# Performance work log

Hardware: AMD Instinct MI355X
Metric: run time of the kernel (lower is better)

## Reference

```python
import jax, jax.numpy as jnp
import numpy as np

N = 50000
E = 800000
D = 128
EPS = 1e-5


def _init_lin(key, d_in, d_out):
    return (jax.random.normal(key, (d_out, d_in), dtype=jnp.float32) / np.sqrt(d_in)).astype(jnp.float32)


def setup_inputs() -> dict:
    key = jax.random.key(0)
    ks = jax.random.split(key, 16)
    x = jax.random.normal(ks[0], (N, D), dtype=jnp.float32)
    edge_index = jax.random.randint(ks[1], (2, E), 0, N, dtype=jnp.int32)
    inp = {"x": x, "edge_index": edge_index}
    # 3 SAGEConv layers: Wl (neighbor/aggr path, with bias), Wr (root path, no bias)
    for i in range(3):
        inp[f"Wl{i}"] = _init_lin(ks[2 + 3 * i], D, D)
        inp[f"bl{i}"] = jnp.zeros((D,), dtype=jnp.float32)
        inp[f"Wr{i}"] = _init_lin(ks[3 + 3 * i], D, D)
    # single LayerNorm (applied after conv0 only, since len(norms)=num_layers-2=1)
    inp["ln_g"] = jnp.ones((D,), dtype=jnp.float32)
    inp["ln_b"] = jnp.zeros((D,), dtype=jnp.float32)
    return inp


def _sage_conv(x, src, dst, Wl, bl, Wr):
    # sum-aggregate source features into destination nodes: [N, D]
    agg = jax.ops.segment_sum(x[src], dst, num_segments=N)
    return agg @ Wl.T + bl + x @ Wr.T


def _layernorm(h, g, b):
    mu = jnp.mean(h, axis=-1, keepdims=True)
    var = jnp.mean(jnp.square(h - mu), axis=-1, keepdims=True)
    return (h - mu) * jax.lax.rsqrt(var + EPS) * g + b


def reference(x, edge_index, Wl0, bl0, Wr0, Wl1, bl1, Wr1, Wl2, bl2, Wr2, ln_g, ln_b):
    src, dst = edge_index[0], edge_index[1]
    # layer 0: conv -> layernorm -> relu (dropout inactive in eval)
    h = _sage_conv(x, src, dst, Wl0, bl0, Wr0)
    h = jax.nn.relu(_layernorm(h, ln_g, ln_b))
    # layer 1: conv -> relu (no norm: i >= len(norms))
    h = jax.nn.relu(_sage_conv(h, src, dst, Wl1, bl1, Wr1))
    # layer 2: final conv, no activation
    return _sage_conv(h, src, dst, Wl2, bl2, Wr2)
```

## Files before the change

### kernel.cpp

```cpp
#include <hip/hip_runtime.h>
#include <hip/hip_bf16.h>

#define NN 50000
#define EE 800000
#define DD 128
#define SLOTS 64
#define PART 6250
#define GEMM_BLOCKS 391
#define PLACE_BLOCKS 4096
#define STRIPE 1563
#define POISON ((int)0xAAAAAAAA)

typedef __attribute__((ext_vector_type(8))) short short8;
typedef __attribute__((ext_vector_type(4))) float floatx4;
typedef __attribute__((ext_vector_type(4))) unsigned short ushort4_t;

__device__ __forceinline__ short f2bf(float f) {
  union { float f; unsigned u; } c; c.f = f;
  unsigned r = c.u + 0x7FFFu + ((c.u >> 16) & 1u);
  return (short)(r >> 16);
}
__device__ __forceinline__ float bf2f(short s) {
  union { unsigned u; float f; } c; c.u = ((unsigned)(unsigned short)s) << 16;
  return c.f;
}
__device__ __forceinline__ unsigned pk(float a, float b) {
  return ((unsigned)(unsigned short)f2bf(a)) | (((unsigned)(unsigned short)f2bf(b)) << 16);
}

__global__ __launch_bounds__(256) void place_k(
    const int* __restrict__ srcE, const int* __restrict__ dstE,
    int* __restrict__ fill, unsigned short* __restrict__ srcSorted,
    const float* __restrict__ W0, const float* __restrict__ W1,
    const float* __restrict__ W2, const float* __restrict__ W3,
    const float* __restrict__ W4, const float* __restrict__ W5,
    short* __restrict__ Wbf, int* __restrict__ Udummy) {
  int b = blockIdx.x;
  if (b < 384) {
    int i = b * 256 + threadIdx.x;
    int mat = i >> 14, local = i & 16383;
    const float* W;
    switch (mat) {
      case 0: W = W0; break;
      case 1: W = W1; break;
      case 2: W = W2; break;
      case 3: W = W3; break;
      case 4: W = W4; break;
      default: W = W5; break;
    }
    int r = local >> 7, c = local & 127;
    int idx = r * DD + (((c >> 3) ^ (r & 15)) << 3) + (c & 7);
    Wbf[(mat << 14) + idx] = f2bf(W[local]);
    if (b == 0 && threadIdx.x < 64) Udummy[threadIdx.x] = 0;
  }
  int p = b & 7;
  int stripe = b >> 3;
  int base = stripe * STRIPE;
  for (int i = threadIdx.x; i < STRIPE; i += 256) {
    int e = base + i;
    if (e < EE) {
      int d = dstE[e];
      int s = srcE[e];
      if ((d & 7) == p) {
        int slot = atomicAdd(&fill[p * PART + (d >> 3)], 1) - POISON;
        if (slot >= 0 && slot < SLOTS)
          srcSorted[(size_t)d * SLOTS + slot] = (unsigned short)s;
      }
    }
  }
}

template <int BF16IN, int VBF16>
__global__ __launch_bounds__(512) void dual_gemm(
    const void* __restrict__ Ain, const short* __restrict__ Wpair,
    const float* __restrict__ bias,
    short* __restrict__ U, void* __restrict__ V)
{
  __shared__ __align__(16) short lw[2 * DD * DD];
  int t = threadIdx.x;
  {
    const short8* gp = (const short8*)Wpair;
    short8* lp = (short8*)lw;
#pragma unroll
    for (int i = 0; i < 8; ++i) lp[t + i * 512] = gp[t + i * 512];
  }

  int wave = t >> 6, lane = t & 63;
  int m = lane & 15, q = lane >> 4;
  int lrow = wave * 16 + m;
  int node = blockIdx.x * 128 + lrow;
  int ar = node < NN ? node : NN - 1;

  short8 af[4];
  if (BF16IN) {
    const short* H = (const short*)Ain + (size_t)ar * DD;
#pragma unroll
    for (int kc = 0; kc < 4; ++kc) af[kc] = *(const short8*)(H + kc * 32 + q * 8);
  } else {
    const floatx4* ap = (const floatx4*)((const float*)Ain + (size_t)ar * DD);
#pragma unroll
    for (int kc = 0; kc < 4; ++kc) {
      floatx4 p0 = ap[kc * 8 + q * 2];
      floatx4 p1 = ap[kc * 8 + q * 2 + 1];
      short8 s;
      s[0] = f2bf(p0[0]); s[1] = f2bf(p0[1]); s[2] = f2bf(p0[2]); s[3] = f2bf(p0[3]);
      s[4] = f2bf(p1[0]); s[5] = f2bf(p1[1]); s[6] = f2bf(p1[2]); s[7] = f2bf(p1[3]);
      af[kc] = s;
    }
  }
  __syncthreads();

  uint2 uacc[8];
  uint2 vaccb[8];
  floatx4 vaccf[8];
#pragma unroll
  for (int ct = 0; ct < 8; ++ct) {
    floatx4 au = {0.f, 0.f, 0.f, 0.f}, av = {0.f, 0.f, 0.f, 0.f};
    int colq = ct * 16 + q * 4;
    const short* pl = &lw[(ct * 16 + m) * DD];
    const short* pr = &lw[DD * DD + (ct * 16 + m) * DD];
#pragma unroll
    for (int kc = 0; kc < 4; ++kc) {
      int pos = (((kc * 4 + q) ^ m) << 3);
      short8 bl_ = *(const short8*)(pl + pos);
      short8 br_ = *(const short8*)(pr + pos);
      au = __builtin_amdgcn_mfma_f32_16x16x32_bf16(bl_, af[kc], au, 0, 0, 0);
      av = __builtin_amdgcn_mfma_f32_16x16x32_bf16(br_, af[kc], av, 0, 0, 0);
    }
    floatx4 bv = *(const floatx4*)(bias + colq);
    uacc[ct].x = pk(au[0], au[1]);
    uacc[ct].y = pk(au[2], au[3]);
    if (VBF16) {
      vaccb[ct].x = pk(av[0] + bv[0], av[1] + bv[1]);
      vaccb[ct].y = pk(av[2] + bv[2], av[3] + bv[3]);
    } else {
      floatx4 vv = {av[0] + bv[0], av[1] + bv[1], av[2] + bv[2], av[3] + bv[3]};
      vaccf[ct] = vv;
    }
  }
  __syncthreads();

  int base = blockIdx.x * 128;
  if (VBF16) {
#pragma unroll
    for (int ct = 0; ct < 8; ++ct) {
      int p = (ct * 4 + q) ^ m;
      *(uint2*)(lw + lrow * 128 + p * 4) = uacc[ct];
      *(uint2*)(lw + 16384 + lrow * 128 + p * 4) = vaccb[ct];
    }
    __syncthreads();
#pragma unroll
    for (int it = 0; it < 8; ++it) {
      int f = it * 512 + t;
      int row = f >> 5, gi = f & 31;
      int nd = base + row;
      if (nd < NN) {
        int p = gi ^ (row & 15);
        *(uint2*)(U + (size_t)nd * DD + gi * 4) =
            *(const uint2*)(lw + row * 128 + p * 4);
        *(uint2*)((short*)V + (size_t)nd * DD + gi * 4) =
            *(const uint2*)(lw + 16384 + row * 128 + p * 4);
      }
    }
  } else {
#pragma unroll
    for (int ct = 0; ct < 8; ++ct) {
      int p = (ct * 4 + q) ^ m;
      *(uint2*)(lw + lrow * 128 + p * 4) = uacc[ct];
    }
    __syncthreads();
#pragma unroll
    for (int it = 0; it < 8; ++it) {
      int f = it * 512 + t;
      int row = f >> 5, gi = f & 31;
      int nd = base + row;
      if (nd < NN) {
        int p = gi ^ (row & 15);
        *(uint2*)(U + (size_t)nd * DD + gi * 4) =
            *(const uint2*)(lw + row * 128 + p * 4);
      }
    }
    __syncthreads();
    float* lf = (float*)lw;
#pragma unroll
    for (int ct = 0; ct < 8; ++ct) {
      int p = (ct * 4 + q) ^ m;
      *(floatx4*)(lf + lrow * 128 + p * 4) = vaccf[ct];
    }
    __syncthreads();
#pragma unroll
    for (int it = 0; it < 8; ++it) {
      int f = it * 512 + t;
      int row = f >> 5, gi = f & 31;
      int nd = base + row;
      if (nd < NN) {
        int p = gi ^ (row & 15);
        *(floatx4*)((float*)V + (size_t)nd * DD + gi * 4) =
            *(const floatx4*)(lf + row * 128 + p * 4);
      }
    }
  }
}

template <int MODE>
__global__ __launch_bounds__(256) void agg_fuse(
    const short* __restrict__ U, const unsigned short* __restrict__ srcSorted,
    const int* __restrict__ fill, const short* __restrict__ Vbf,
    float* __restrict__ Vf, short* __restrict__ H,
    const float* __restrict__ g, const float* __restrict__ b)
{
  int node = blockIdx.x * 4 + (threadIdx.x >> 6);
  int lane = threadIdx.x & 63;
  int c = lane & 15, r = lane >> 4;
  int coff = c << 3;

  int deg = fill[(node & 7) * PART + (node >> 3)] - POISON;
  deg = deg < SLOTS ? deg : SLOTS;
  const unsigned short* seg = srcSorted + (size_t)node * SLOTS;

  float acc[8] = {0.f, 0.f, 0.f, 0.f, 0.f, 0.f, 0.f, 0.f};
  int nbatch = (deg + 15) >> 4;
  for (int bb = 0; bb < nbatch; ++bb) {
    int s0 = bb * 16 + (r << 2);
    ushort4_t idx = *(const ushort4_t*)(seg + s0);
    int ra0 = (s0 + 0) < deg ? (int)idx[0] : NN;
    int ra1 = (s0 + 1) < deg ? (int)idx[1] : NN;
    int ra2 = (s0 + 2) < deg ? (int)idx[2] : NN;
    int ra3 = (s0 + 3) < deg ? (int)idx[3] : NN;
    short8 v0 = *(const short8*)(U + ((size_t)ra0 << 7) + coff);
    short8 v1 = *(const short8*)(U + ((size_t)ra1 << 7) + coff);
    short8 v2 = *(const short8*)(U + ((size_t)ra2 << 7) + coff);
    short8 v3 = *(const short8*)(U + ((size_t)ra3 << 7) + coff);
#pragma unroll
    for (int j = 0; j < 8; ++j)
      acc[j] += (bf2f(v0[j]) + bf2f(v1[j])) + (bf2f(v2[j]) + bf2f(v3[j]));
  }
#pragma unroll
  for (int j = 0; j < 8; ++j) {
    acc[j] += __shfl_xor(acc[j], 16, 64);
    acc[j] += __shfl_xor(acc[j], 32, 64);
  }

  if (MODE == 0) {
    short8 vv = *(const short8*)(Vbf + ((size_t)node << 7) + coff);
#pragma unroll
    for (int j = 0; j < 8; ++j) acc[j] += bf2f(vv[j]);
    float s = 0.f;
#pragma unroll
    for (int j = 0; j < 8; ++j) s += acc[j];
    s += __shfl_xor(s, 1, 64); s += __shfl_xor(s, 2, 64);
    s += __shfl_xor(s, 4, 64); s += __shfl_xor(s, 8, 64);
    float mu = s * (1.0f / 128.0f);
    float q2 = 0.f;
#pragma unroll
    for (int j = 0; j < 8; ++j) { float d = acc[j] - mu; q2 += d * d; }
    q2 += __shfl_xor(q2, 1, 64); q2 += __shfl_xor(q2, 2, 64);
    q2 += __shfl_xor(q2, 4, 64); q2 += __shfl_xor(q2, 8, 64);
    float rstd = rsqrtf(q2 * (1.0f / 128.0f) + 1e-5f);
    floatx4 g0 = *(const floatx4*)(g + coff), g1 = *(const floatx4*)(g + coff + 4);
    floatx4 b0 = *(const floatx4*)(b + coff), b1 = *(const floatx4*)(b + coff + 4);
    float o[8];
#pragma unroll
    for (int j = 0; j < 4; ++j) {
      o[j]     = (acc[j]     - mu) * rstd * g0[j] + b0[j];
      o[4 + j] = (acc[4 + j] - mu) * rstd * g1[j] + b1[j];
    }
#pragma unroll
    for (int j = 0; j < 8; ++j) o[j] = o[j] > 0.f ? o[j] : 0.f;
    if (r == 0) {
      uint4 pkt = {pk(o[0], o[1]), pk(o[2], o[3]), pk(o[4], o[5]), pk(o[6], o[7])};
      *(uint4*)(H + ((size_t)node << 7) + coff) = pkt;
    }
  } else if (MODE == 1) {
    if (r == 0) {
      short8 vv = *(const short8*)(Vbf + ((size_t)node << 7) + coff);
#pragma unroll
      for (int j = 0; j < 8; ++j) {
        acc[j] += bf2f(vv[j]);
        acc[j] = acc[j] > 0.f ? acc[j] : 0.f;
      }
      uint4 pkt = {pk(acc[0], acc[1]), pk(acc[2], acc[3]),
                   pk(acc[4], acc[5]), pk(acc[6], acc[7])};
      *(uint4*)(H + ((size_t)node << 7) + coff) = pkt;
    }
  } else {
    if (r == 0) {
      float* vp = Vf + ((size_t)node << 7) + coff;
      floatx4 a0 = ((const floatx4*)vp)[0];
      floatx4 a1 = ((const floatx4*)vp)[1];
      floatx4 o0 = {acc[0] + a0[0], acc[1] + a0[1], acc[2] + a0[2], acc[3] + a0[3]};
      floatx4 o1 = {acc[4] + a1[0], acc[5] + a1[1], acc[6] + a1[2], acc[7] + a1[3]};
      ((floatx4*)vp)[0] = o0;
      ((floatx4*)vp)[1] = o1;
    }
  }
}

extern "C" void kernel_launch(void* const* d_in, const int* in_sizes, int n_in,
                              void* d_out, int out_size, void* d_ws, size_t ws_size,
                              hipStream_t stream) {
  const float* x   = (const float*)d_in[0];
  const int*   ei  = (const int*)d_in[1];
  const int* src = ei;
  const int* dst = ei + EE;
  const float* Wl0 = (const float*)d_in[2];
  const float* bl0 = (const float*)d_in[3];
  const float* Wr0 = (const float*)d_in[4];
  const float* Wl1 = (const float*)d_in[5];
  const float* bl1 = (const float*)d_in[6];
  const float* Wr1 = (const float*)d_in[7];
  const float* Wl2 = (const float*)d_in[8];
  const float* bl2 = (const float*)d_in[9];
  const float* Wr2 = (const float*)d_in[10];
  const float* lng = (const float*)d_in[11];
  const float* lnb = (const float*)d_in[12];

  short* Vbf = (short*)d_out;
  float* Vf  = (float*)d_out;

  short* U   = (short*)d_ws;
  short* Hb  = U + (size_t)(NN + 1) * DD;
  short* Wbf = Hb + (size_t)NN * DD;
  unsigned short* srcS = (unsigned short*)(Wbf + 6 * DD * DD);
  int* fill  = (int*)(srcS + (size_t)NN * SLOTS);

  dim3 blk(256);
  dim3 gblk(512);

  place_k<<<PLACE_BLOCKS, blk, 0, stream>>>(src, dst, fill, srcS,
                                            Wl0, Wr0, Wl1, Wr1, Wl2, Wr2,
                                            Wbf, (int*)(U + (size_t)NN * DD));

  dual_gemm<0, 1><<<GEMM_BLOCKS, gblk, 0, stream>>>(
      x, Wbf + 0 * 2 * DD * DD, bl0, U, Vbf);
  agg_fuse<0><<<NN / 4, blk, 0, stream>>>(U, srcS, fill, Vbf, Vf, Hb, lng, lnb);

  dual_gemm<1, 1><<<GEMM_BLOCKS, gblk, 0, stream>>>(
      Hb, Wbf + 1 * 2 * DD * DD, bl1, U, Vbf);
  agg_fuse<1><<<NN / 4, blk, 0, stream>>>(U, srcS, fill, Vbf, Vf, Hb, lng, lnb);

  dual_gemm<1, 0><<<GEMM_BLOCKS, gblk, 0, stream>>>(
      Hb, Wbf + 2 * 2 * DD * DD, bl2, U, Vf);
  agg_fuse<2><<<NN / 4, blk, 0, stream>>>(U, srcS, fill, Vbf, Vf, Hb, lng, lnb);
}
```

Baseline: 266.5 us.

## Fuse layer-0 GEMM with edge placement kernel and use nontemporal loads

```diff
diff --git a/kernel.cpp b/kernel.cpp
--- a/kernel.cpp
+++ b/kernel.cpp
@@ -7,8 +7,8 @@
 #define SLOTS 64
 #define PART 6250
 #define GEMM_BLOCKS 391
-#define PLACE_BLOCKS 4096
-#define STRIPE 1563
+#define PLACE_BLOCKS 2048
+#define STRIPE2 3125
 #define POISON ((int)0xAAAAAAAA)
 
 typedef __attribute__((ext_vector_type(8))) short short8;
@@ -28,51 +28,124 @@
   return ((unsigned)(unsigned short)f2bf(a)) | (((unsigned)(unsigned short)f2bf(b)) << 16);
 }
 
-__global__ __launch_bounds__(256) void place_k(
+__global__ __launch_bounds__(512) void gemm0_place(
+    const float* __restrict__ x,
+    const float* __restrict__ Wl0, const float* __restrict__ Wr0,
+    const float* __restrict__ bias,
+    short* __restrict__ U, short* __restrict__ Vbf,
     const int* __restrict__ srcE, const int* __restrict__ dstE,
     int* __restrict__ fill, unsigned short* __restrict__ srcSorted,
-    const float* __restrict__ W0, const float* __restrict__ W1,
-    const float* __restrict__ W2, const float* __restrict__ W3,
-    const float* __restrict__ W4, const float* __restrict__ W5,
-    short* __restrict__ Wbf, int* __restrict__ Udummy) {
-  int b = blockIdx.x;
-  if (b < 384) {
-    int i = b * 256 + threadIdx.x;
-    int mat = i >> 14, local = i & 16383;
-    const float* W;
-    switch (mat) {
-      case 0: W = W0; break;
-      case 1: W = W1; break;
-      case 2: W = W2; break;
-      case 3: W = W3; break;
-      case 4: W = W4; break;
-      default: W = W5; break;
-    }
-    int r = local >> 7, c = local & 127;
-    int idx = r * DD + (((c >> 3) ^ (r & 15)) << 3) + (c & 7);
-    Wbf[(mat << 14) + idx] = f2bf(W[local]);
-    if (b == 0 && threadIdx.x < 64) Udummy[threadIdx.x] = 0;
-  }
-  int p = b & 7;
-  int stripe = b >> 3;
-  int base = stripe * STRIPE;
-  for (int i = threadIdx.x; i < STRIPE; i += 256) {
-    int e = base + i;
-    if (e < EE) {
-      int d = dstE[e];
-      int s = srcE[e];
+    const float* __restrict__ Wl1, const float* __restrict__ Wr1,
+    const float* __restrict__ Wl2, const float* __restrict__ Wr2,
+    short* __restrict__ Wbf, int* __restrict__ Udummy)
+{
+  __shared__ __align__(16) short lw[2 * DD * DD];
+  int t = threadIdx.x;
+
+  if (blockIdx.x >= GEMM_BLOCKS) {
+    int b = blockIdx.x - GEMM_BLOCKS;
+    if (b < 128) {
+      int i = b * 512 + t;
+      int mat = i >> 14, local = i & 16383;
+      const float* W = (mat == 0) ? Wl1 : (mat == 1) ? Wr1 : (mat == 2) ? Wl2 : Wr2;
+      int r = local >> 7, c = local & 127;
+      int idx = r * DD + (((c >> 3) ^ (r & 15)) << 3) + (c & 7);
+      Wbf[(mat << 14) + idx] = f2bf(W[local]);
+      if (b == 0 && t < 64) Udummy[t] = 0;
+    }
+    int p = b & 7;
+    int stripe = b >> 3;
+    int base = stripe * STRIPE2;
+    for (int i = t; i < STRIPE2; i += 512) {
+      int e = base + i;
+      int d = __builtin_nontemporal_load(dstE + e);
+      int s = __builtin_nontemporal_load(srcE + e);
       if ((d & 7) == p) {
         int slot = atomicAdd(&fill[p * PART + (d >> 3)], 1) - POISON;
         if (slot >= 0 && slot < SLOTS)
           srcSorted[(size_t)d * SLOTS + slot] = (unsigned short)s;
       }
     }
-  }
-}
-
-template <int BF16IN, int VBF16>
+    return;
+  }
+
+  for (int i = t; i < DD * DD; i += 512) {
+    int r = i >> 7, c = i & 127;
+    int idx = r * DD + (((c >> 3) ^ (r & 15)) << 3) + (c & 7);
+    lw[idx] = f2bf(Wl0[i]);
+    lw[DD * DD + idx] = f2bf(Wr0[i]);
+  }
+
+  int wave = t >> 6, lane = t & 63;
+  int m = lane & 15, q = lane >> 4;
+  int lrow = wave * 16 + m;
+  int node = blockIdx.x * 128 + lrow;
+  int ar = node < NN ? node : NN - 1;
+
+  short8 af[4];
+  {
+    const floatx4* ap = (const floatx4*)(x + (size_t)ar * DD);
+#pragma unroll
+    for (int kc = 0; kc < 4; ++kc) {
+      floatx4 p0 = ap[kc * 8 + q * 2];
+      floatx4 p1 = ap[kc * 8 + q * 2 + 1];
+      short8 s;
+      s[0] = f2bf(p0[0]); s[1] = f2bf(p0[1]); s[2] = f2bf(p0[2]); s[3] = f2bf(p0[3]);
+      s[4] = f2bf(p1[0]); s[5] = f2bf(p1[1]); s[6] = f2bf(p1[2]); s[7] = f2bf(p1[3]);
+      af[kc] = s;
+    }
+  }
+  __syncthreads();
+
+  uint2 uacc[8], vaccb[8];
+#pragma unroll
+  for (int ct = 0; ct < 8; ++ct) {
+    floatx4 au = {0.f, 0.f, 0.f, 0.f}, av = {0.f, 0.f, 0.f, 0.f};
+    int colq = ct * 16 + q * 4;
+    const short* pl = &lw[(ct * 16 + m) * DD];
+    const short* pr = &lw[DD * DD + (ct * 16 + m) * DD];
+#pragma unroll
+    for (int kc = 0; kc < 4; ++kc) {
+      int pos = (((kc * 4 + q) ^ m) << 3);
+      short8 bl_ = *(const short8*)(pl + pos);
+      short8 br_ = *(const short8*)(pr + pos);
+      au = __builtin_amdgcn_mfma_f32_16x16x32_bf16(bl_, af[kc], au, 0, 0, 0);
+      av = __builtin_amdgcn_mfma_f32_16x16x32_bf16(br_, af[kc], av, 0, 0, 0);
+    }
+    floatx4 bv = *(const floatx4*)(bias + colq);
+    uacc[ct].x = pk(au[0], au[1]);
+    uacc[ct].y = pk(au[2], au[3]);
+    vaccb[ct].x = pk(av[0] + bv[0], av[1] + bv[1]);
+    vaccb[ct].y = pk(av[2] + bv[2], av[3] + bv[3]);
+  }
+  __syncthreads();
+
+  int base = blockIdx.x * 128;
+#pragma unroll
+  for (int ct = 0; ct < 8; ++ct) {
+    int p = (ct * 4 + q) ^ m;
+    *(uint2*)(lw + lrow * 128 + p * 4) = uacc[ct];
+    *(uint2*)(lw + 16384 + lrow * 128 + p * 4) = vaccb[ct];
+  }
+  __syncthreads();
+#pragma unroll
+  for (int it = 0; it < 8; ++it) {
+    int f = it * 512 + t;
+    int row = f >> 5, gi = f & 31;
+    int nd = base + row;
+    if (nd < NN) {
+      int p = gi ^ (row & 15);
+      *(uint2*)(U + (size_t)nd * DD + gi * 4) =
+          *(const uint2*)(lw + row * 128 + p * 4);
+      *(uint2*)(Vbf + (size_t)nd * DD + gi * 4) =
+          *(const uint2*)(lw + 16384 + row * 128 + p * 4);
+    }
+  }
+}
+
+template <int VBF16>
 __global__ __launch_bounds__(512) void dual_gemm(
-    const void* __restrict__ Ain, const short* __restrict__ Wpair,
+    const short* __restrict__ Ain, const short* __restrict__ Wpair,
     const float* __restrict__ bias,
     short* __restrict__ U, void* __restrict__ V)
 {
@@ -92,26 +165,14 @@
   int ar = node < NN ? node : NN - 1;
 
   short8 af[4];
-  if (BF16IN) {
-    const short* H = (const short*)Ain + (size_t)ar * DD;
+  {
+    const short* H = Ain + (size_t)ar * DD;
 #pragma unroll
     for (int kc = 0; kc < 4; ++kc) af[kc] = *(const short8*)(H + kc * 32 + q * 8);
-  } else {
-    const floatx4* ap = (const floatx4*)((const float*)Ain + (size_t)ar * DD);
-#pragma unroll
-    for (int kc = 0; kc < 4; ++kc) {
-      floatx4 p0 = ap[kc * 8 + q * 2];
-      floatx4 p1 = ap[kc * 8 + q * 2 + 1];
-      short8 s;
-      s[0] = f2bf(p0[0]); s[1] = f2bf(p0[1]); s[2] = f2bf(p0[2]); s[3] = f2bf(p0[3]);
-      s[4] = f2bf(p1[0]); s[5] = f2bf(p1[1]); s[6] = f2bf(p1[2]); s[7] = f2bf(p1[3]);
-      af[kc] = s;
-    }
   }
   __syncthreads();
 
-  uint2 uacc[8];
-  uint2 vaccb[8];
+  uint2 uacc[8], vaccb[8];
   floatx4 vaccf[8];
 #pragma unroll
   for (int ct = 0; ct < 8; ++ct) {
@@ -222,7 +283,7 @@
   int nbatch = (deg + 15) >> 4;
   for (int bb = 0; bb < nbatch; ++bb) {
     int s0 = bb * 16 + (r << 2);
-    ushort4_t idx = *(const ushort4_t*)(seg + s0);
+    ushort4_t idx = __builtin_nontemporal_load((const ushort4_t*)(seg + s0));
     int ra0 = (s0 + 0) < deg ? (int)idx[0] : NN;
     int ra1 = (s0 + 1) < deg ? (int)idx[1] : NN;
     int ra2 = (s0 + 2) < deg ? (int)idx[2] : NN;
@@ -321,25 +382,22 @@
   short* U   = (short*)d_ws;
   short* Hb  = U + (size_t)(NN + 1) * DD;
   short* Wbf = Hb + (size_t)NN * DD;
-  unsigned short* srcS = (unsigned short*)(Wbf + 6 * DD * DD);
+  unsigned short* srcS = (unsigned short*)(Wbf + 4 * DD * DD);
   int* fill  = (int*)(srcS + (size_t)NN * SLOTS);
 
   dim3 blk(256);
   dim3 gblk(512);
 
-  place_k<<<PLACE_BLOCKS, blk, 0, stream>>>(src, dst, fill, srcS,
-                                            Wl0, Wr0, Wl1, Wr1, Wl2, Wr2,
-                                            Wbf, (int*)(U + (size_t)NN * DD));
-
-  dual_gemm<0, 1><<<GEMM_BLOCKS, gblk, 0, stream>>>(
-      x, Wbf + 0 * 2 * DD * DD, bl0, U, Vbf);
+  gemm0_place<<<GEMM_BLOCKS + PLACE_BLOCKS, gblk, 0, stream>>>(
+      x, Wl0, Wr0, bl0, U, Vbf, src, dst, fill, srcS,
+      Wl1, Wr1, Wl2, Wr2, Wbf, (int*)(U + (size_t)NN * DD));
   agg_fuse<0><<<NN / 4, blk, 0, stream>>>(U, srcS, fill, Vbf, Vf, Hb, lng, lnb);
 
-  dual_gemm<1, 1><<<GEMM_BLOCKS, gblk, 0, stream>>>(
-      Hb, Wbf + 1 * 2 * DD * DD, bl1, U, Vbf);
+  dual_gemm<1><<<GEMM_BLOCKS, gblk, 0, stream>>>(
+      Hb, Wbf + 0 * 2 * DD * DD, bl1, U, Vbf);
   agg_fuse<1><<<NN / 4, blk, 0, stream>>>(U, srcS, fill, Vbf, Vf, Hb, lng, lnb);
 
-  dual_gemm<1, 0><<<GEMM_BLOCKS, gblk, 0, stream>>>(
-      Hb, Wbf + 2 * 2 * DD * DD, bl2, U, Vf);
+  dual_gemm<0><<<GEMM_BLOCKS, gblk, 0, stream>>>(
+      Hb, Wbf + 1 * 2 * DD * DD, bl2, U, Vf);
   agg_fuse<2><<<NN / 4, blk, 0, stream>>>(U, srcS, fill, Vbf, Vf, Hb, lng, lnb);
 }
```

Result: slower. 294.1 us (+10.4%).

## Fuse all phases into one cooperative persistent kernel with grid syncs

Applied to the files above, without the earlier changes.

```diff
diff --git a/kernel.cpp b/kernel.cpp
--- a/kernel.cpp
+++ b/kernel.cpp
@@ -1,14 +1,16 @@
 #include <hip/hip_runtime.h>
 #include <hip/hip_bf16.h>
+#include <hip/hip_cooperative_groups.h>
+
+namespace cg = cooperative_groups;
 
 #define NN 50000
 #define EE 800000
 #define DD 128
 #define SLOTS 64
 #define PART 6250
-#define GEMM_BLOCKS 391
-#define PLACE_BLOCKS 4096
-#define STRIPE 1563
+#define NT 782
+#define NG 6250
 #define POISON ((int)0xAAAAAAAA)
 
 typedef __attribute__((ext_vector_type(8))) short short8;
@@ -28,75 +30,61 @@
   return ((unsigned)(unsigned short)f2bf(a)) | (((unsigned)(unsigned short)f2bf(b)) << 16);
 }
 
-__global__ __launch_bounds__(256) void place_k(
-    const int* __restrict__ srcE, const int* __restrict__ dstE,
-    int* __restrict__ fill, unsigned short* __restrict__ srcSorted,
-    const float* __restrict__ W0, const float* __restrict__ W1,
-    const float* __restrict__ W2, const float* __restrict__ W3,
-    const float* __restrict__ W4, const float* __restrict__ W5,
-    short* __restrict__ Wbf, int* __restrict__ Udummy) {
-  int b = blockIdx.x;
-  if (b < 384) {
-    int i = b * 256 + threadIdx.x;
+struct MP {
+  const float *x, *Wl0, *bl0, *Wr0, *Wl1, *bl1, *Wr1, *Wl2, *bl2, *Wr2, *lng, *lnb;
+  const int *src, *dst;
+  short *U, *Hb, *Wbf, *Vbf;
+  float *Vf;
+  unsigned short *srcS;
+  int *fill;
+  int *Udummy;
+};
+
+__device__ __forceinline__ void dev_prep(const MP& P, int start, int stride) {
+  for (int i = start; i < 4 * DD * DD; i += stride) {
     int mat = i >> 14, local = i & 16383;
-    const float* W;
-    switch (mat) {
-      case 0: W = W0; break;
-      case 1: W = W1; break;
-      case 2: W = W2; break;
-      case 3: W = W3; break;
-      case 4: W = W4; break;
-      default: W = W5; break;
-    }
+    const float* W = mat == 0 ? P.Wl1 : mat == 1 ? P.Wr1 : mat == 2 ? P.Wl2 : P.Wr2;
     int r = local >> 7, c = local & 127;
-    int idx = r * DD + (((c >> 3) ^ (r & 15)) << 3) + (c & 7);
-    Wbf[(mat << 14) + idx] = f2bf(W[local]);
-    if (b == 0 && threadIdx.x < 64) Udummy[threadIdx.x] = 0;
-  }
-  int p = b & 7;
-  int stripe = b >> 3;
-  int base = stripe * STRIPE;
-  for (int i = threadIdx.x; i < STRIPE; i += 256) {
+    P.Wbf[(mat << 14) + r * DD + (((c >> 3) ^ (r & 15)) << 3) + (c & 7)] = f2bf(W[local]);
+  }
+}
+
+__device__ __forceinline__ void dev_place(const MP& P, int pb, int npb) {
+  int p = pb & 7;
+  int S = npb >> 3;
+  int len = (EE + S - 1) / S;
+  int base = (pb >> 3) * len;
+  for (int i = threadIdx.x; i < len; i += 512) {
     int e = base + i;
     if (e < EE) {
-      int d = dstE[e];
-      int s = srcE[e];
+      int d = __builtin_nontemporal_load(P.dst + e);
+      int s = __builtin_nontemporal_load(P.src + e);
       if ((d & 7) == p) {
-        int slot = atomicAdd(&fill[p * PART + (d >> 3)], 1) - POISON;
+        int slot = atomicAdd(&P.fill[p * PART + (d >> 3)], 1) - POISON;
         if (slot >= 0 && slot < SLOTS)
-          srcSorted[(size_t)d * SLOTS + slot] = (unsigned short)s;
+          P.srcS[(size_t)d * SLOTS + slot] = (unsigned short)s;
       }
     }
   }
 }
 
-template <int BF16IN, int VBF16>
-__global__ __launch_bounds__(512) void dual_gemm(
-    const void* __restrict__ Ain, const short* __restrict__ Wpair,
-    const float* __restrict__ bias,
-    short* __restrict__ U, void* __restrict__ V)
+template <int AFP32, int VBF16, int SELFW>
+__device__ __forceinline__ void dev_gemm_tile(
+    const void* Ain, const float* WlF, const float* WrF,
+    const short* Wpair, const float* bias,
+    short* U, void* V, short* lw, int tile)
 {
-  __shared__ __align__(16) short lw[2 * DD * DD];
   int t = threadIdx.x;
-  {
-    const short8* gp = (const short8*)Wpair;
-    short8* lp = (short8*)lw;
-#pragma unroll
-    for (int i = 0; i < 8; ++i) lp[t + i * 512] = gp[t + i * 512];
-  }
-
   int wave = t >> 6, lane = t & 63;
   int m = lane & 15, q = lane >> 4;
-  int lrow = wave * 16 + m;
-  int node = blockIdx.x * 128 + lrow;
+  int hi = wave >> 2, pi = wave & 3;
+  int node = tile * 64 + pi * 16 + m;
   int ar = node < NN ? node : NN - 1;
+  int lrow = pi * 16 + m;
+  int base = tile * 64;
 
   short8 af[4];
-  if (BF16IN) {
-    const short* H = (const short*)Ain + (size_t)ar * DD;
-#pragma unroll
-    for (int kc = 0; kc < 4; ++kc) af[kc] = *(const short8*)(H + kc * 32 + q * 8);
-  } else {
+  if (AFP32) {
     const floatx4* ap = (const floatx4*)((const float*)Ain + (size_t)ar * DD);
 #pragma unroll
     for (int kc = 0; kc < 4; ++kc) {
@@ -107,130 +95,154 @@
       s[4] = f2bf(p1[0]); s[5] = f2bf(p1[1]); s[6] = f2bf(p1[2]); s[7] = f2bf(p1[3]);
       af[kc] = s;
     }
-  }
-  __syncthreads();
-
-  uint2 uacc[8];
-  uint2 vaccb[8];
-  floatx4 vaccf[8];
-#pragma unroll
-  for (int ct = 0; ct < 8; ++ct) {
-    floatx4 au = {0.f, 0.f, 0.f, 0.f}, av = {0.f, 0.f, 0.f, 0.f};
-    int colq = ct * 16 + q * 4;
+  } else {
+    const short* H = (const short*)Ain + (size_t)ar * DD;
+#pragma unroll
+    for (int kc = 0; kc < 4; ++kc) af[kc] = *(const short8*)(H + kc * 32 + q * 8);
+  }
+
+  if (SELFW) {
+    for (int i = t; i < DD * DD; i += 512) {
+      int r = i >> 7, c = i & 127;
+      lw[r * DD + (((c >> 3) ^ (r & 15)) << 3) + (c & 7)] = f2bf(WlF[i]);
+    }
+  } else {
+    const short8* gp = (const short8*)Wpair;
+    short8* lp = (short8*)lw;
+#pragma unroll
+    for (int i = 0; i < 4; ++i) lp[t + i * 512] = gp[t + i * 512];
+  }
+  __syncthreads();
+
+  uint2 uacc[4];
+#pragma unroll
+  for (int c2 = 0; c2 < 4; ++c2) {
+    int ct = hi * 4 + c2;
+    floatx4 au = {0.f, 0.f, 0.f, 0.f};
     const short* pl = &lw[(ct * 16 + m) * DD];
-    const short* pr = &lw[DD * DD + (ct * 16 + m) * DD];
 #pragma unroll
     for (int kc = 0; kc < 4; ++kc) {
       int pos = (((kc * 4 + q) ^ m) << 3);
-      short8 bl_ = *(const short8*)(pl + pos);
-      short8 br_ = *(const short8*)(pr + pos);
-      au = __builtin_amdgcn_mfma_f32_16x16x32_bf16(bl_, af[kc], au, 0, 0, 0);
-      av = __builtin_amdgcn_mfma_f32_16x16x32_bf16(br_, af[kc], av, 0, 0, 0);
-    }
-    floatx4 bv = *(const floatx4*)(bias + colq);
-    uacc[ct].x = pk(au[0], au[1]);
-    uacc[ct].y = pk(au[2], au[3]);
+      au = __builtin_amdgcn_mfma_f32_16x16x32_bf16(*(const short8*)(pl + pos), af[kc], au, 0, 0, 0);
+    }
+    uacc[c2].x = pk(au[0], au[1]);
+    uacc[c2].y = pk(au[2], au[3]);
+  }
+  __syncthreads();
+#pragma unroll
+  for (int c2 = 0; c2 < 4; ++c2) {
+    int g = (hi * 4 + c2) * 4 + q;
+    *(uint2*)(lw + lrow * 128 + ((g ^ m) << 2)) = uacc[c2];
+  }
+  __syncthreads();
+#pragma unroll
+  for (int it = 0; it < 4; ++it) {
+    int f = it * 512 + t;
+    int row = f >> 5, gi = f & 31;
+    int nd = base + row;
+    if (nd < NN)
+      *(uint2*)(U + (size_t)nd * DD + gi * 4) =
+          *(const uint2*)(lw + row * 128 + ((gi ^ (row & 15)) << 2));
+  }
+  __syncthreads();
+
+  if (SELFW) {
+    for (int i = t; i < DD * DD; i += 512) {
+      int r = i >> 7, c = i & 127;
+      lw[r * DD + (((c >> 3) ^ (r & 15)) << 3) + (c & 7)] = f2bf(WrF[i]);
+    }
+  } else {
+    const short8* gp = (const short8*)(Wpair + DD * DD);
+    short8* lp = (short8*)lw;
+#pragma unroll
+    for (int i = 0; i < 4; ++i) lp[t + i * 512] = gp[t + i * 512];
+  }
+  __syncthreads();
+
+  uint2 vb[4];
+  floatx4 vf[4];
+#pragma unroll
+  for (int c2 = 0; c2 < 4; ++c2) {
+    int ct = hi * 4 + c2;
+    floatx4 av = {0.f, 0.f, 0.f, 0.f};
+    const short* pr = &lw[(ct * 16 + m) * DD];
+#pragma unroll
+    for (int kc = 0; kc < 4; ++kc) {
+      int pos = (((kc * 4 + q) ^ m) << 3);
+      av = __builtin_amdgcn_mfma_f32_16x16x32_bf16(*(const short8*)(pr + pos), af[kc], av, 0, 0, 0);
+    }
+    floatx4 bv = *(const floatx4*)(bias + ct * 16 + q * 4);
     if (VBF16) {
-      vaccb[ct].x = pk(av[0] + bv[0], av[1] + bv[1]);
-      vaccb[ct].y = pk(av[2] + bv[2], av[3] + bv[3]);
+      vb[c2].x = pk(av[0] + bv[0], av[1] + bv[1]);
+      vb[c2].y = pk(av[2] + bv[2], av[3] + bv[3]);
     } else {
       floatx4 vv = {av[0] + bv[0], av[1] + bv[1], av[2] + bv[2], av[3] + bv[3]};
-      vaccf[ct] = vv;
-    }
-  }
-  __syncthreads();
-
-  int base = blockIdx.x * 128;
+      vf[c2] = vv;
+    }
+  }
+  __syncthreads();
   if (VBF16) {
 #pragma unroll
-    for (int ct = 0; ct < 8; ++ct) {
-      int p = (ct * 4 + q) ^ m;
-      *(uint2*)(lw + lrow * 128 + p * 4) = uacc[ct];
-      *(uint2*)(lw + 16384 + lrow * 128 + p * 4) = vaccb[ct];
+    for (int c2 = 0; c2 < 4; ++c2) {
+      int g = (hi * 4 + c2) * 4 + q;
+      *(uint2*)(lw + lrow * 128 + ((g ^ m) << 2)) = vb[c2];
     }
     __syncthreads();
 #pragma unroll
-    for (int it = 0; it < 8; ++it) {
+    for (int it = 0; it < 4; ++it) {
       int f = it * 512 + t;
       int row = f >> 5, gi = f & 31;
       int nd = base + row;
-      if (nd < NN) {
-        int p = gi ^ (row & 15);
-        *(uint2*)(U + (size_t)nd * DD + gi * 4) =
-            *(const uint2*)(lw + row * 128 + p * 4);
+      if (nd < NN)
         *(uint2*)((short*)V + (size_t)nd * DD + gi * 4) =
-            *(const uint2*)(lw + 16384 + row * 128 + p * 4);
-      }
-    }
-  } else {
-#pragma unroll
-    for (int ct = 0; ct < 8; ++ct) {
-      int p = (ct * 4 + q) ^ m;
-      *(uint2*)(lw + lrow * 128 + p * 4) = uacc[ct];
+            *(const uint2*)(lw + row * 128 + ((gi ^ (row & 15)) << 2));
+    }
+  } else {
+    float* lf = (float*)lw;
+#pragma unroll
+    for (int c2 = 0; c2 < 4; ++c2) {
+      int g = (hi * 4 + c2) * 4 + q;
+      *(floatx4*)(lf + lrow * 128 + (g ^ m) * 4) = vf[c2];
     }
     __syncthreads();
 #pragma unroll
-    for (int it = 0; it < 8; ++it) {
+    for (int it = 0; it < 4; ++it) {
       int f = it * 512 + t;
       int row = f >> 5, gi = f & 31;
       int nd = base + row;
-      if (nd < NN) {
-        int p = gi ^ (row & 15);
-        *(uint2*)(U + (size_t)nd * DD + gi * 4) =
-            *(const uint2*)(lw + row * 128 + p * 4);
-      }
-    }
-    __syncthreads();
-    float* lf = (float*)lw;
-#pragma unroll
-    for (int ct = 0; ct < 8; ++ct) {
-      int p = (ct * 4 + q) ^ m;
-      *(floatx4*)(lf + lrow * 128 + p * 4) = vaccf[ct];
-    }
-    __syncthreads();
-#pragma unroll
-    for (int it = 0; it < 8; ++it) {
-      int f = it * 512 + t;
-      int row = f >> 5, gi = f & 31;
-      int nd = base + row;
-      if (nd < NN) {
-        int p = gi ^ (row & 15);
+      if (nd < NN)
         *(floatx4*)((float*)V + (size_t)nd * DD + gi * 4) =
-            *(const floatx4*)(lf + row * 128 + p * 4);
-      }
-    }
-  }
+            *(const floatx4*)(lf + row * 128 + (gi ^ (row & 15)) * 4);
+    }
+  }
+  __syncthreads();
 }
 
 template <int MODE>
-__global__ __launch_bounds__(256) void agg_fuse(
-    const short* __restrict__ U, const unsigned short* __restrict__ srcSorted,
-    const int* __restrict__ fill, const short* __restrict__ Vbf,
-    float* __restrict__ Vf, short* __restrict__ H,
-    const float* __restrict__ g, const float* __restrict__ b)
-{
-  int node = blockIdx.x * 4 + (threadIdx.x >> 6);
-  int lane = threadIdx.x & 63;
+__device__ __forceinline__ void dev_agg(const MP& P, int g) {
+  int t = threadIdx.x;
+  int wave = t >> 6, lane = t & 63;
+  int node = g * 8 + wave;
   int c = lane & 15, r = lane >> 4;
   int coff = c << 3;
 
-  int deg = fill[(node & 7) * PART + (node >> 3)] - POISON;
+  int deg = P.fill[(node & 7) * PART + (node >> 3)] - POISON;
   deg = deg < SLOTS ? deg : SLOTS;
-  const unsigned short* seg = srcSorted + (size_t)node * SLOTS;
+  const unsigned short* seg = P.srcS + (size_t)node * SLOTS;
 
   float acc[8] = {0.f, 0.f, 0.f, 0.f, 0.f, 0.f, 0.f, 0.f};
   int nbatch = (deg + 15) >> 4;
   for (int bb = 0; bb < nbatch; ++bb) {
     int s0 = bb * 16 + (r << 2);
-    ushort4_t idx = *(const ushort4_t*)(seg + s0);
+    ushort4_t idx = __builtin_nontemporal_load((const ushort4_t*)(seg + s0));
     int ra0 = (s0 + 0) < deg ? (int)idx[0] : NN;
     int ra1 = (s0 + 1) < deg ? (int)idx[1] : NN;
     int ra2 = (s0 + 2) < deg ? (int)idx[2] : NN;
     int ra3 = (s0 + 3) < deg ? (int)idx[3] : NN;
-    short8 v0 = *(const short8*)(U + ((size_t)ra0 << 7) + coff);
-    short8 v1 = *(const short8*)(U + ((size_t)ra1 << 7) + coff);
-    short8 v2 = *(const short8*)(U + ((size_t)ra2 << 7) + coff);
-    short8 v3 = *(const short8*)(U + ((size_t)ra3 << 7) + coff);
+    short8 v0 = *(const short8*)(P.U + ((size_t)ra0 << 7) + coff);
+    short8 v1 = *(const short8*)(P.U + ((size_t)ra1 << 7) + coff);
+    short8 v2 = *(const short8*)(P.U + ((size_t)ra2 << 7) + coff);
+    short8 v3 = *(const short8*)(P.U + ((size_t)ra3 << 7) + coff);
 #pragma unroll
     for (int j = 0; j < 8; ++j)
       acc[j] += (bf2f(v0[j]) + bf2f(v1[j])) + (bf2f(v2[j]) + bf2f(v3[j]));
@@ -242,7 +254,7 @@
   }
 
   if (MODE == 0) {
-    short8 vv = *(const short8*)(Vbf + ((size_t)node << 7) + coff);
+    short8 vv = *(const short8*)(P.Vbf + ((size_t)node << 7) + coff);
 #pragma unroll
     for (int j = 0; j < 8; ++j) acc[j] += bf2f(vv[j]);
     float s = 0.f;
@@ -257,8 +269,8 @@
     q2 += __shfl_xor(q2, 1, 64); q2 += __shfl_xor(q2, 2, 64);
     q2 += __shfl_xor(q2, 4, 64); q2 += __shfl_xor(q2, 8, 64);
     float rstd = rsqrtf(q2 * (1.0f / 128.0f) + 1e-5f);
-    floatx4 g0 = *(const floatx4*)(g + coff), g1 = *(const floatx4*)(g + coff + 4);
-    floatx4 b0 = *(const floatx4*)(b + coff), b1 = *(const floatx4*)(b + coff + 4);
+    floatx4 g0 = *(const floatx4*)(P.lng + coff), g1 = *(const floatx4*)(P.lng + coff + 4);
+    floatx4 b0 = *(const floatx4*)(P.lnb + coff), b1 = *(const floatx4*)(P.lnb + coff + 4);
     float o[8];
 #pragma unroll
     for (int j = 0; j < 4; ++j) {
@@ -269,11 +281,11 @@
     for (int j = 0; j < 8; ++j) o[j] = o[j] > 0.f ? o[j] : 0.f;
     if (r == 0) {
       uint4 pkt = {pk(o[0], o[1]), pk(o[2], o[3]), pk(o[4], o[5]), pk(o[6], o[7])};
-      *(uint4*)(H + ((size_t)node << 7) + coff) = pkt;
+      *(uint4*)(P.Hb + ((size_t)node << 7) + coff) = pkt;
     }
   } else if (MODE == 1) {
     if (r == 0) {
-      short8 vv = *(const short8*)(Vbf + ((size_t)node << 7) + coff);
+      short8 vv = *(const short8*)(P.Vbf + ((size_t)node << 7) + coff);
 #pragma unroll
       for (int j = 0; j < 8; ++j) {
         acc[j] += bf2f(vv[j]);
@@ -281,11 +293,11 @@
       }
       uint4 pkt = {pk(acc[0], acc[1]), pk(acc[2], acc[3]),
                    pk(acc[4], acc[5]), pk(acc[6], acc[7])};
-      *(uint4*)(H + ((size_t)node << 7) + coff) = pkt;
+      *(uint4*)(P.Hb + ((size_t)node << 7) + coff) = pkt;
     }
   } else {
     if (r == 0) {
-      float* vp = Vf + ((size_t)node << 7) + coff;
+      float* vp = P.Vf + ((size_t)node << 7) + coff;
       floatx4 a0 = ((const floatx4*)vp)[0];
       floatx4 a1 = ((const floatx4*)vp)[1];
       floatx4 o0 = {acc[0] + a0[0], acc[1] + a0[1], acc[2] + a0[2], acc[3] + a0[3]};
@@ -296,50 +308,92 @@
   }
 }
 
+__global__ __launch_bounds__(512) void mega(MP P) {
+  __shared__ __align__(16) short lw[DD * DD];
+  cg::grid_group gg = cg::this_grid();
+  int nb = gridDim.x;
+
+  for (int tile = blockIdx.x; tile < NT; tile += nb)
+    dev_gemm_tile<1, 1, 1>(P.x, P.Wl0, P.Wr0, nullptr, P.bl0, P.U, P.Vbf, lw, tile);
+  dev_prep(P, blockIdx.x * 512 + threadIdx.x, nb * 512);
+  if (blockIdx.x == 0 && threadIdx.x < 64) P.Udummy[threadIdx.x] = 0;
+  dev_place(P, blockIdx.x, nb);
+  gg.sync();
+  for (int g = blockIdx.x; g < NG; g += nb) dev_agg<0>(P, g);
+  gg.sync();
+  for (int tile = blockIdx.x; tile < NT; tile += nb)
+    dev_gemm_tile<0, 1, 0>(P.Hb, nullptr, nullptr, P.Wbf, P.bl1, P.U, P.Vbf, lw, tile);
+  gg.sync();
+  for (int g = blockIdx.x; g < NG; g += nb) dev_agg<1>(P, g);
+  gg.sync();
+  for (int tile = blockIdx.x; tile < NT; tile += nb)
+    dev_gemm_tile<0, 0, 0>(P.Hb, nullptr, nullptr, P.Wbf + 2 * DD * DD, P.bl2, P.U, P.Vf, lw, tile);
+  gg.sync();
+  for (int g = blockIdx.x; g < NG; g += nb) dev_agg<2>(P, g);
+}
+
+__global__ __launch_bounds__(512) void k_phase0(MP P) {
+  __shared__ __align__(16) short lw[DD * DD];
+  int nb = gridDim.x;
+  for (int tile = blockIdx.x; tile < NT; tile += nb)
+    dev_gemm_tile<1, 1, 1>(P.x, P.Wl0, P.Wr0, nullptr, P.bl0, P.U, P.Vbf, lw, tile);
+  dev_prep(P, blockIdx.x * 512 + threadIdx.x, nb * 512);
+  if (blockIdx.x == 0 && threadIdx.x < 64) P.Udummy[threadIdx.x] = 0;
+  dev_place(P, blockIdx.x, nb);
+}
+__global__ __launch_bounds__(512) void k_gemm1(MP P) {
+  __shared__ __align__(16) short lw[DD * DD];
+  dev_gemm_tile<0, 1, 0>(P.Hb, nullptr, nullptr, P.Wbf, P.bl1, P.U, P.Vbf, lw, blockIdx.x);
+}
+__global__ __launch_bounds__(512) void k_gemm2(MP P) {
+  __shared__ __align__(16) short lw[DD * DD];
+  dev_gemm_tile<0, 0, 0>(P.Hb, nullptr, nullptr, P.Wbf + 2 * DD * DD, P.bl2, P.U, P.Vf, lw, blockIdx.x);
+}
+template <int MODE>
+__global__ __launch_bounds__(512) void k_agg(MP P) { dev_agg<MODE>(P, blockIdx.x); }
+
 extern "C" void kernel_launch(void* const* d_in, const int* in_sizes, int n_in,
                               void* d_out, int out_size, void* d_ws, size_t ws_size,
                               hipStream_t stream) {
-  const float* x   = (const float*)d_in[0];
-  const int*   ei  = (const int*)d_in[1];
-  const int* src = ei;
-  const int* dst = ei + EE;
-  const float* Wl0 = (const float*)d_in[2];
-  const float* bl0 = (const float*)d_in[3];
-  const float* Wr0 = (const float*)d_in[4];
-  const float* Wl1 = (const float*)d_in[5];
-  const float* bl1 = (const float*)d_in[6];
-  const float* Wr1 = (const float*)d_in[7];
-  const float* Wl2 = (const float*)d_in[8];
-  const float* bl2 = (const float*)d_in[9];
-  const float* Wr2 = (const float*)d_in[10];
-  const float* lng = (const float*)d_in[11];
-  const float* lnb = (const float*)d_in[12];
-
-  short* Vbf = (short*)d_out;
-  float* Vf  = (float*)d_out;
-
-  short* U   = (short*)d_ws;
-  short* Hb  = U + (size_t)(NN + 1) * DD;
-  short* Wbf = Hb + (size_t)NN * DD;
-  unsigned short* srcS = (unsigned short*)(Wbf + 6 * DD * DD);
-  int* fill  = (int*)(srcS + (size_t)NN * SLOTS);
-
-  dim3 blk(256);
-  dim3 gblk(512);
-
-  place_k<<<PLACE_BLOCKS, blk, 0, stream>>>(src, dst, fill, srcS,
-                                            Wl0, Wr0, Wl1, Wr1, Wl2, Wr2,
-                                            Wbf, (int*)(U + (size_t)NN * DD));
-
-  dual_gemm<0, 1><<<GEMM_BLOCKS, gblk, 0, stream>>>(
-      x, Wbf + 0 * 2 * DD * DD, bl0, U, Vbf);
-  agg_fuse<0><<<NN / 4, blk, 0, stream>>>(U, srcS, fill, Vbf, Vf, Hb, lng, lnb);
-
-  dual_gemm<1, 1><<<GEMM_BLOCKS, gblk, 0, stream>>>(
-      Hb, Wbf + 1 * 2 * DD * DD, bl1, U, Vbf);
-  agg_fuse<1><<<NN / 4, blk, 0, stream>>>(U, srcS, fill, Vbf, Vf, Hb, lng, lnb);
-
-  dual_gemm<1, 0><<<GEMM_BLOCKS, gblk, 0, stream>>>(
-      Hb, Wbf + 2 * 2 * DD * DD, bl2, U, Vf);
-  agg_fuse<2><<<NN / 4, blk, 0, stream>>>(U, srcS, fill, Vbf, Vf, Hb, lng, lnb);
-}
+  MP P;
+  P.x   = (const float*)d_in[0];
+  const int* ei = (const int*)d_in[1];
+  P.src = ei; P.dst = ei + EE;
+  P.Wl0 = (const float*)d_in[2];  P.bl0 = (const float*)d_in[3];
+  P.Wr0 = (const float*)d_in[4];
+  P.Wl1 = (const float*)d_in[5];  P.bl1 = (const float*)d_in[6];
+  P.Wr1 = (const float*)d_in[7];
+  P.Wl2 = (const float*)d_in[8];  P.bl2 = (const float*)d_in[9];
+  P.Wr2 = (const float*)d_in[10];
+  P.lng = (const float*)d_in[11]; P.lnb = (const float*)d_in[12];
+
+  P.Vbf = (short*)d_out;
+  P.Vf  = (float*)d_out;
+
+  P.U   = (short*)d_ws;
+  P.Hb  = P.U + (size_t)(NN + 1) * DD;
+  P.Wbf = P.Hb + (size_t)NN * DD;
+  P.srcS = (unsigned short*)(P.Wbf + 4 * DD * DD);
+  P.fill = (int*)(P.srcS + (size_t)NN * SLOTS);
+  P.Udummy = (int*)(P.U + (size_t)NN * DD);
+
+  int nbcu = 0;
+  hipError_t qe = hipOccupancyMaxActiveBlocksPerMultiprocessor(&nbcu, (const void*)mega, 512, 0);
+  int grid = (qe == hipSuccess && nbcu > 0) ? nbcu * 256 : 512;
+  if (grid > 1024) grid = 1024;
+  grid &= ~7;
+  if (grid < 8) grid = 8;
+
+  void* args[] = {(void*)&P};
+  hipError_t le = hipLaunchCooperativeKernel((const void*)mega, dim3(grid), dim3(512),
+                                             args, 0, stream);
+  if (le != hipSuccess) {
+    dim3 blk(512);
+    k_phase0<<<1024, blk, 0, stream>>>(P);
+    k_agg<0><<<NG, blk, 0, stream>>>(P);
+    k_gemm1<<<NT, blk, 0, stream>>>(P);
+    k_agg<1><<<NG, blk, 0, stream>>>(P);
+    k_gemm2<<<NT, blk, 0, stream>>>(P);
+    k_agg<2><<<NG, blk, 0, stream>>>(P);
+  }
+}
```

Measured after the change: 588.5 us. 121% more time.
